# Optimization experiments

Hardware: AMD Instinct MI355X
Metric: run time of the kernel (lower is better)

The kernel has to match this reference:

```python
import jax, jax.numpy as jnp
import numpy as np

B, T, I, H, FUT = 16384, 50, 6, 128, 30


def setup_inputs() -> dict:
    key = jax.random.key(0)
    ks = jax.random.split(key, 10)
    bound = 1.0 / np.sqrt(H)
    u = lambda k, shape: jax.random.uniform(k, shape, jnp.float32, -bound, bound)
    return {
        "history": jax.random.normal(ks[0], (B, T, I), jnp.float32),
        # GRU weights (PyTorch layout: gates stacked [r, z, n])
        "w_ih": u(ks[1], (3 * H, I)),
        "w_hh": u(ks[2], (3 * H, H)),
        "b_ih": u(ks[3], (3 * H,)),
        "b_hh": u(ks[4], (3 * H,)),
        # MLP head: Linear(H,H) -> ReLU -> Linear(H,I)
        "w1": u(ks[5], (H, H)),
        "b1": u(ks[6], (H,)),
        "w2": u(ks[7], (I, H)),
        "b2": u(ks[8], (I,)),
    }


def _gru_cell(h, x, w_ih, w_hh, b_ih, b_hh):
    # PyTorch GRU cell: gates ordered r, z, n
    gi = x @ w_ih.T + b_ih          # (B, 3H)
    gh = h @ w_hh.T + b_hh          # (B, 3H)
    i_r, i_z, i_n = jnp.split(gi, 3, axis=-1)
    h_r, h_z, h_n = jnp.split(gh, 3, axis=-1)
    r = jax.nn.sigmoid(i_r + h_r)
    z = jax.nn.sigmoid(i_z + h_z)
    n = jnp.tanh(i_n + r * h_n)
    return (1.0 - z) * n + z * h


def reference(history, w_ih, w_hh, b_ih, b_hh, w1, b1, w2, b2):
    # --- encode history: scan GRU over time ---
    h0 = jnp.zeros((history.shape[0], H), history.dtype)

    def enc_step(h, x_t):
        return _gru_cell(h, x_t, w_ih, w_hh, b_ih, b_hh), None

    h_last, _ = jax.lax.scan(enc_step, h0, jnp.swapaxes(history, 0, 1))  # (B, H)

    def head(h):
        return jax.nn.relu(h @ w1.T + b1) @ w2.T + b2  # (B, I)

    def dec_step(carry, _):
        h, x = carry
        h = _gru_cell(h, x, w_ih, w_hh, b_ih, b_hh)
        x = head(h)
        return (h, x), x

    x0 = history[:, -1]  # (B, I)
    _, preds = jax.lax.scan(dec_step, (h_last, x0), None, length=FUT)  # (FUT, B, I)
    return jnp.swapaxes(preds, 0, 1)  # (B, FUT, I)
```

## Files before the change

### kernel.cpp

```cpp
#include <hip/hip_runtime.h>

typedef _Float16 half8 __attribute__((ext_vector_type(8)));
typedef float f32x4 __attribute__((ext_vector_type(4)));

#define ROWS 32
#define HP 136
#define HBUFSZ (ROWS * HP)
#define LOG2E 1.442695041f
#define MFMA(a, b, c) __builtin_amdgcn_mfma_f32_16x16x32_f16((a), (b), (c), 0, 0, 0)

__global__ __launch_bounds__(512, 4)
void traj_gru(const float* __restrict__ history,
              const float* __restrict__ w_ih, const float* __restrict__ w_hh,
              const float* __restrict__ b_ih, const float* __restrict__ b_hh,
              const float* __restrict__ w1, const float* __restrict__ b1,
              const float* __restrict__ w2, const float* __restrict__ b2,
              float* __restrict__ out)
{
    __shared__ __align__(16) _Float16 hbuf[2 * HBUFSZ];
    __shared__ __align__(16) _Float16 xhist[50 * ROWS * 8];
    __shared__ __align__(16) _Float16 xdec[ROWS * 8];
    __shared__ __align__(16) _Float16 a1s[ROWS * HP];
    __shared__ __align__(16) _Float16 w2f[4 * 4 * 16 * 8];

    const int tid  = threadIdx.x;
    const int wave = tid >> 6;
    const int lane = tid & 63;
    const int ln16 = lane & 15;
    const int q    = lane >> 4;
    const int rowbase = blockIdx.x * ROWS;
    const int cbase = wave * 16;

    for (int i = tid; i < 2 * HBUFSZ; i += 512) hbuf[i] = (_Float16)0;
    for (int i = tid; i < 50 * ROWS * 8; i += 512) xhist[i] = (_Float16)0;
    for (int i = tid; i < ROWS * 8; i += 512) xdec[i] = (_Float16)0;
    for (int i = tid; i < 4 * 4 * 16 * 8; i += 512) w2f[i] = (_Float16)0;
    __syncthreads();

    for (int idx = tid; idx < ROWS * 300; idx += 512) {
        int r = idx / 300, rem = idx - r * 300;
        int t = rem / 6, c = rem - t * 6;
        xhist[(t * ROWS + r) * 8 + c] = (_Float16)history[(rowbase + r) * 300 + rem];
    }
    for (int idx = tid; idx < 50 * ROWS; idx += 512)
        xhist[idx * 8 + 6] = (_Float16)1.0f;
    for (int idx = tid; idx < ROWS; idx += 512)
        xdec[idx * 8 + 6] = (_Float16)1.0f;
    for (int idx = tid; idx < 6 * 128; idx += 512) {
        int n = idx >> 7, k = idx & 127;
        int kt = k >> 5, qq = (k >> 3) & 3, j = k & 7;
        w2f[((kt * 4 + qq) * 16 + n) * 8 + j] = (_Float16)w2[n * 128 + k];
    }

    half8 Bh[3][4];
    #pragma unroll
    for (int g = 0; g < 3; ++g) {
        float sc = (g < 2) ? -LOG2E : -2.0f * LOG2E;
        #pragma unroll
        for (int kt = 0; kt < 4; ++kt) {
            int n = g * 128 + cbase + ln16;
            const float* p = w_hh + n * 128 + kt * 32 + q * 8;
            half8 v;
            #pragma unroll
            for (int j = 0; j < 8; ++j) v[j] = (_Float16)(p[j] * sc);
            Bh[g][kt] = v;
        }
    }
    half8 Bi[3];
    #pragma unroll
    for (int g = 0; g < 3; ++g) {
        float sc = (g < 2) ? -LOG2E : -2.0f * LOG2E;
        int n = g * 128 + cbase + ln16;
        half8 v;
        #pragma unroll
        for (int j = 0; j < 8; ++j) v[j] = (_Float16)0.0f;
        if (q == 0) {
            #pragma unroll
            for (int j = 0; j < 6; ++j) v[j] = (_Float16)(w_ih[n * 6 + j] * sc);
            v[6] = (_Float16)((b_ih[n] + (g < 2 ? b_hh[n] : 0.0f)) * sc);
        }
        Bi[g] = v;
    }
    const float bhn = b_hh[256 + cbase + ln16] * (-2.0f * LOG2E);
    half8 Bw1[4];
    #pragma unroll
    for (int kt = 0; kt < 4; ++kt) {
        int n = cbase + ln16;
        const float* p = w1 + n * 128 + kt * 32 + q * 8;
        half8 v;
        #pragma unroll
        for (int j = 0; j < 8; ++j) v[j] = (_Float16)p[j];
        Bw1[kt] = v;
    }
    const float b1r = b1[cbase + ln16];
    const float b2r = (ln16 < 6) ? b2[ln16] : 0.0f;

    float hp[2][4] = {};

    __syncthreads();

    auto gru_step = [&](int p, const _Float16* xp) {
        const _Float16* hb = hbuf + p * HBUFSZ;
        _Float16*       hn = hbuf + (p ^ 1) * HBUFSZ;
        #pragma unroll
        for (int mt = 0; mt < 2; ++mt) {
            const _Float16* rp = hb + (mt * 16 + ln16) * HP + q * 8;
            half8 Ax = {0,0,0,0,0,0,0,0};
            if (q == 0) Ax = *(const half8*)(xp + (mt * 16 + ln16) * 8);
            f32x4 ar = {0,0,0,0}, az = {0,0,0,0}, ah = {0,0,0,0}, an = {0,0,0,0};
            half8 Acur = *(const half8*)(rp);
            #pragma unroll
            for (int kt = 0; kt < 4; ++kt) {
                half8 Anext;
                if (kt < 3) Anext = *(const half8*)(rp + (kt + 1) * 32);
                ar = MFMA(Acur, Bh[0][kt], ar);
                az = MFMA(Acur, Bh[1][kt], az);
                ah = MFMA(Acur, Bh[2][kt], ah);
                Acur = Anext;
            }
            ar = MFMA(Ax, Bi[0], ar);
            az = MFMA(Ax, Bi[1], az);
            an = MFMA(Ax, Bi[2], an);
            _Float16* wp = hn + (mt * 16 + q * 4) * HP + cbase + ln16;
            #pragma unroll
            for (int i = 0; i < 4; ++i) {
                float r = __builtin_amdgcn_rcpf(1.0f + __builtin_amdgcn_exp2f(ar[i]));
                float z = __builtin_amdgcn_rcpf(1.0f + __builtin_amdgcn_exp2f(az[i]));
                float t = an[i] + r * (ah[i] + bhn);
                float n = 2.0f * __builtin_amdgcn_rcpf(1.0f + __builtin_amdgcn_exp2f(t)) - 1.0f;
                float h = n + z * (hp[mt][i] - n);
                hp[mt][i] = h;
                wp[i * HP] = (_Float16)h;
            }
        }
        __syncthreads();
    };

    auto head_step = [&](int f, int p) {
        const _Float16* hb = hbuf + p * HBUFSZ;
        #pragma unroll
        for (int mt = 0; mt < 2; ++mt) {
            const _Float16* rp = hb + (mt * 16 + ln16) * HP + q * 8;
            f32x4 a = {0,0,0,0};
            half8 Acur = *(const half8*)(rp);
            #pragma unroll
            for (int kt = 0; kt < 4; ++kt) {
                half8 Anext;
                if (kt < 3) Anext = *(const half8*)(rp + (kt + 1) * 32);
                a = MFMA(Acur, Bw1[kt], a);
                Acur = Anext;
            }
            _Float16* wp = a1s + (mt * 16 + q * 4) * HP + cbase + ln16;
            #pragma unroll
            for (int i = 0; i < 4; ++i) {
                float v = a[i] + b1r;
                v = v > 0.0f ? v : 0.0f;
                wp[i * HP] = (_Float16)v;
            }
        }
        __syncthreads();
        if (wave < 2) {
            f32x4 o = {0,0,0,0};
            #pragma unroll
            for (int kt = 0; kt < 4; ++kt) {
                half8 Aa = *(const half8*)&a1s[(wave * 16 + ln16) * HP + kt * 32 + q * 8];
                half8 Bw = *(const half8*)&w2f[((kt * 4 + q) * 16 + ln16) * 8];
                o = MFMA(Aa, Bw, o);
            }
            if (ln16 < 6) {
                #pragma unroll
                for (int i = 0; i < 4; ++i) {
                    int row = wave * 16 + q * 4 + i;
                    float v = o[i] + b2r;
                    out[(rowbase + row) * 180 + f * 6 + ln16] = v;
                    xdec[row * 8 + ln16] = (_Float16)v;
                }
            }
        }
        __syncthreads();
    };

    int p = 0;
    #pragma unroll 1
    for (int t = 0; t < 50; ++t) { gru_step(p, xhist + t * ROWS * 8); p ^= 1; }
    #pragma unroll 1
    for (int f = 0; f < 30; ++f) {
        gru_step(p, f == 0 ? xhist + 49 * ROWS * 8 : xdec);
        p ^= 1;
        head_step(f, p);
    }
}

extern "C" void kernel_launch(void* const* d_in, const int* in_sizes, int n_in,
                              void* d_out, int out_size, void* d_ws, size_t ws_size,
                              hipStream_t stream) {
    (void)in_sizes; (void)n_in; (void)d_ws; (void)ws_size; (void)out_size;
    traj_gru<<<dim3(16384 / ROWS), dim3(512), 0, stream>>>(
        (const float*)d_in[0], (const float*)d_in[1], (const float*)d_in[2],
        (const float*)d_in[3], (const float*)d_in[4], (const float*)d_in[5],
        (const float*)d_in[6], (const float*)d_in[7], (const float*)d_in[8],
        (float*)d_out);
}
```

Measured before the change: 287.4 us.

## Switch GRU to 32x32x16 MFMA with 4 waves and transposed operand roles

Moves the GRU recurrence from 8 waves of 16x16x32 MFMA to 4 waves of 32x32x16 MFMA. Weights become the A operand and the hidden state the B operand, so each wave computes 32 hidden dims for all 32 rows. It also folds b_hn into an extra MFMA, merges the z and tanh reciprocals into a single rcp, and packs h stores into half4 writes. The head now reloads w1 from global memory each step and adds a staggered s_sleep per block. Register pressure rises with 8 k-tiles of weights per gate and 16-wide accumulators, and w1 is reloaded from global on every decode step.

```diff
diff --git a/kernel.cpp b/kernel.cpp
--- a/kernel.cpp
+++ b/kernel.cpp
@@ -1,15 +1,19 @@
 #include <hip/hip_runtime.h>
 
 typedef _Float16 half8 __attribute__((ext_vector_type(8)));
+typedef _Float16 half4 __attribute__((ext_vector_type(4)));
 typedef float f32x4 __attribute__((ext_vector_type(4)));
+typedef float f32x16 __attribute__((ext_vector_type(16)));
+typedef int int4v __attribute__((ext_vector_type(4)));
 
 #define ROWS 32
 #define HP 136
-#define HBUFSZ (ROWS * HP)
+#define HB (ROWS * HP)
 #define LOG2E 1.442695041f
-#define MFMA(a, b, c) __builtin_amdgcn_mfma_f32_16x16x32_f16((a), (b), (c), 0, 0, 0)
-
-__global__ __launch_bounds__(512, 4)
+#define MFMA32(a,b,c) __builtin_amdgcn_mfma_f32_32x32x16_f16((a),(b),(c),0,0,0)
+#define MFMA16(a,b,c) __builtin_amdgcn_mfma_f32_16x16x32_f16((a),(b),(c),0,0,0)
+
+__global__ __launch_bounds__(256, 2)
 void traj_gru(const float* __restrict__ history,
               const float* __restrict__ w_ih, const float* __restrict__ w_hh,
               const float* __restrict__ b_ih, const float* __restrict__ b_hh,
@@ -17,155 +21,193 @@
               const float* __restrict__ w2, const float* __restrict__ b2,
               float* __restrict__ out)
 {
-    __shared__ __align__(16) _Float16 hbuf[2 * HBUFSZ];
-    __shared__ __align__(16) _Float16 xhist[50 * ROWS * 8];
+    __shared__ __align__(16) _Float16 hbuf[2 * HB];
+    __shared__ __align__(16) _Float16 xhist[50 * ROWS * 6];
     __shared__ __align__(16) _Float16 xdec[ROWS * 8];
-    __shared__ __align__(16) _Float16 a1s[ROWS * HP];
     __shared__ __align__(16) _Float16 w2f[4 * 4 * 16 * 8];
 
     const int tid  = threadIdx.x;
     const int wave = tid >> 6;
     const int lane = tid & 63;
+    const int l31  = lane & 31;
+    const int q2   = lane >> 5;
     const int ln16 = lane & 15;
     const int q    = lane >> 4;
     const int rowbase = blockIdx.x * ROWS;
-    const int cbase = wave * 16;
-
-    for (int i = tid; i < 2 * HBUFSZ; i += 512) hbuf[i] = (_Float16)0;
-    for (int i = tid; i < 50 * ROWS * 8; i += 512) xhist[i] = (_Float16)0;
-    for (int i = tid; i < ROWS * 8; i += 512) xdec[i] = (_Float16)0;
-    for (int i = tid; i < 4 * 4 * 16 * 8; i += 512) w2f[i] = (_Float16)0;
+    const int dim0 = wave * 32 + l31;
+
+    for (int i = tid; i < 2 * HB; i += 256) hbuf[i] = (_Float16)0;
+    for (int i = tid; i < ROWS * 8; i += 256) xdec[i] = (_Float16)0;
+    for (int i = tid; i < 4 * 4 * 16 * 8; i += 256) w2f[i] = (_Float16)0;
     __syncthreads();
-
-    for (int idx = tid; idx < ROWS * 300; idx += 512) {
+    for (int idx = tid; idx < ROWS * 300; idx += 256) {
         int r = idx / 300, rem = idx - r * 300;
         int t = rem / 6, c = rem - t * 6;
-        xhist[(t * ROWS + r) * 8 + c] = (_Float16)history[(rowbase + r) * 300 + rem];
-    }
-    for (int idx = tid; idx < 50 * ROWS; idx += 512)
-        xhist[idx * 8 + 6] = (_Float16)1.0f;
-    for (int idx = tid; idx < ROWS; idx += 512)
-        xdec[idx * 8 + 6] = (_Float16)1.0f;
-    for (int idx = tid; idx < 6 * 128; idx += 512) {
+        xhist[(t * ROWS + r) * 6 + c] = (_Float16)history[(rowbase + r) * 300 + rem];
+    }
+    if (tid < ROWS) { xdec[tid * 8 + 6] = (_Float16)1.0f; xdec[tid * 8 + 7] = (_Float16)1.0f; }
+    for (int idx = tid; idx < 6 * 128; idx += 256) {
         int n = idx >> 7, k = idx & 127;
         int kt = k >> 5, qq = (k >> 3) & 3, j = k & 7;
         w2f[((kt * 4 + qq) * 16 + n) * 8 + j] = (_Float16)w2[n * 128 + k];
     }
 
-    half8 Bh[3][4];
+    half8 Wg[3][8];
     #pragma unroll
     for (int g = 0; g < 3; ++g) {
         float sc = (g < 2) ? -LOG2E : -2.0f * LOG2E;
         #pragma unroll
-        for (int kt = 0; kt < 4; ++kt) {
-            int n = g * 128 + cbase + ln16;
-            const float* p = w_hh + n * 128 + kt * 32 + q * 8;
+        for (int kt = 0; kt < 8; ++kt) {
+            const float* p = w_hh + (g * 128 + dim0) * 128 + kt * 16 + q2 * 8;
             half8 v;
             #pragma unroll
             for (int j = 0; j < 8; ++j) v[j] = (_Float16)(p[j] * sc);
-            Bh[g][kt] = v;
-        }
-    }
-    half8 Bi[3];
+            Wg[g][kt] = v;
+        }
+    }
+    half8 Wx[3];
     #pragma unroll
     for (int g = 0; g < 3; ++g) {
         float sc = (g < 2) ? -LOG2E : -2.0f * LOG2E;
-        int n = g * 128 + cbase + ln16;
-        half8 v;
-        #pragma unroll
-        for (int j = 0; j < 8; ++j) v[j] = (_Float16)0.0f;
-        if (q == 0) {
-            #pragma unroll
-            for (int j = 0; j < 6; ++j) v[j] = (_Float16)(w_ih[n * 6 + j] * sc);
-            v[6] = (_Float16)((b_ih[n] + (g < 2 ? b_hh[n] : 0.0f)) * sc);
-        }
-        Bi[g] = v;
-    }
-    const float bhn = b_hh[256 + cbase + ln16] * (-2.0f * LOG2E);
-    half8 Bw1[4];
-    #pragma unroll
-    for (int kt = 0; kt < 4; ++kt) {
-        int n = cbase + ln16;
-        const float* p = w1 + n * 128 + kt * 32 + q * 8;
-        half8 v;
-        #pragma unroll
-        for (int j = 0; j < 8; ++j) v[j] = (_Float16)p[j];
-        Bw1[kt] = v;
-    }
-    const float b1r = b1[cbase + ln16];
+        half8 v = {0,0,0,0,0,0,0,0};
+        if (q2 == 0) {
+            #pragma unroll
+            for (int j = 0; j < 6; ++j) v[j] = (_Float16)(w_ih[(g * 128 + dim0) * 6 + j] * sc);
+            float b = (g == 0) ? (b_ih[dim0] + b_hh[dim0])
+                    : (g == 1) ? (b_ih[128 + dim0] + b_hh[128 + dim0])
+                               : b_ih[256 + dim0];
+            v[6] = (_Float16)(b * sc);
+        }
+        Wx[g] = v;
+    }
+    half8 Wbh = {0,0,0,0,0,0,0,0};
+    if (q2 == 0) Wbh[7] = (_Float16)(b_hh[256 + dim0] * (-2.0f * LOG2E));
+
     const float b2r = (ln16 < 6) ? b2[ln16] : 0.0f;
 
-    float hp[2][4] = {};
+    float hp[16] = {};
 
     __syncthreads();
 
-    auto gru_step = [&](int p, const _Float16* xp) {
-        const _Float16* hb = hbuf + p * HBUFSZ;
-        _Float16*       hn = hbuf + (p ^ 1) * HBUFSZ;
-        #pragma unroll
-        for (int mt = 0; mt < 2; ++mt) {
-            const _Float16* rp = hb + (mt * 16 + ln16) * HP + q * 8;
-            half8 Ax = {0,0,0,0,0,0,0,0};
-            if (q == 0) Ax = *(const half8*)(xp + (mt * 16 + ln16) * 8);
-            f32x4 ar = {0,0,0,0}, az = {0,0,0,0}, ah = {0,0,0,0}, an = {0,0,0,0};
-            half8 Acur = *(const half8*)(rp);
-            #pragma unroll
-            for (int kt = 0; kt < 4; ++kt) {
-                half8 Anext;
-                if (kt < 3) Anext = *(const half8*)(rp + (kt + 1) * 32);
-                ar = MFMA(Acur, Bh[0][kt], ar);
-                az = MFMA(Acur, Bh[1][kt], az);
-                ah = MFMA(Acur, Bh[2][kt], ah);
-                Acur = Anext;
-            }
-            ar = MFMA(Ax, Bi[0], ar);
-            az = MFMA(Ax, Bi[1], az);
-            an = MFMA(Ax, Bi[2], an);
-            _Float16* wp = hn + (mt * 16 + q * 4) * HP + cbase + ln16;
+    {
+        int ph = blockIdx.x & 3;
+        for (int i = 0; i < ph; ++i) __builtin_amdgcn_s_sleep(13);
+    }
+
+    auto gru_step = [&](int p, int t, bool enc) {
+        const _Float16* hb = hbuf + p * HB;
+        _Float16*       hn = hbuf + (p ^ 1) * HB;
+
+        half8 Bx;
+        if (enc) {
+            int4v d = {0, 0, 0, 0};
+            if (q2 == 0) {
+                const int* xi = (const int*)xhist;
+                int base = (t * ROWS + l31) * 3;
+                d[0] = xi[base]; d[1] = xi[base + 1]; d[2] = xi[base + 2];
+                d[3] = 0x3C003C00;
+            }
+            Bx = __builtin_bit_cast(half8, d);
+        } else {
+            half8 z = {0,0,0,0,0,0,0,0};
+            Bx = (q2 == 0) ? *(const half8*)(xdec + l31 * 8) : z;
+        }
+
+        f32x16 ar = {0,0,0,0,0,0,0,0,0,0,0,0,0,0,0,0};
+        f32x16 az = ar, ah = ar, an = ar;
+        const _Float16* rp = hb + l31 * HP + q2 * 8;
+
+        half8 Bf[4];
+        #pragma unroll
+        for (int kt = 0; kt < 4; ++kt) Bf[kt] = *(const half8*)(rp + kt * 16);
+        #pragma unroll
+        for (int kt = 0; kt < 4; ++kt) {
+            ar = MFMA32(Wg[0][kt], Bf[kt], ar);
+            az = MFMA32(Wg[1][kt], Bf[kt], az);
+            ah = MFMA32(Wg[2][kt], Bf[kt], ah);
+        }
+        #pragma unroll
+        for (int kt = 0; kt < 4; ++kt) Bf[kt] = *(const half8*)(rp + (kt + 4) * 16);
+        #pragma unroll
+        for (int kt = 0; kt < 4; ++kt) {
+            ar = MFMA32(Wg[0][kt + 4], Bf[kt], ar);
+            az = MFMA32(Wg[1][kt + 4], Bf[kt], az);
+            ah = MFMA32(Wg[2][kt + 4], Bf[kt], ah);
+        }
+        ar = MFMA32(Wx[0], Bx, ar);
+        az = MFMA32(Wx[1], Bx, az);
+        an = MFMA32(Wx[2], Bx, an);
+        ah = MFMA32(Wbh, Bx, ah);
+
+        #pragma unroll
+        for (int rq = 0; rq < 4; ++rq) {
+            half4 hv;
             #pragma unroll
             for (int i = 0; i < 4; ++i) {
-                float r = __builtin_amdgcn_rcpf(1.0f + __builtin_amdgcn_exp2f(ar[i]));
-                float z = __builtin_amdgcn_rcpf(1.0f + __builtin_amdgcn_exp2f(az[i]));
-                float t = an[i] + r * (ah[i] + bhn);
-                float n = 2.0f * __builtin_amdgcn_rcpf(1.0f + __builtin_amdgcn_exp2f(t)) - 1.0f;
-                float h = n + z * (hp[mt][i] - n);
-                hp[mt][i] = h;
-                wp[i * HP] = (_Float16)h;
-            }
+                int ri = rq * 4 + i;
+                float er = __builtin_amdgcn_exp2f(ar[ri]);
+                float r  = __builtin_amdgcn_rcpf(1.0f + er);
+                float tt = __builtin_fmaf(r, ah[ri], an[ri]);
+                float et = __builtin_amdgcn_exp2f(tt);
+                float ez = __builtin_amdgcn_exp2f(az[ri]);
+                float d1 = 1.0f + et;
+                float rd = __builtin_amdgcn_rcpf(d1 * (1.0f + ez));
+                float t1 = __builtin_fmaf(-et, ez, ez);
+                float nm = __builtin_fmaf(hp[ri], d1, t1);
+                float h  = nm * rd;
+                hp[ri] = h;
+                hv[i] = (_Float16)h;
+            }
+            *(half4*)(hn + l31 * HP + wave * 32 + rq * 8 + q2 * 4) = hv;
         }
         __syncthreads();
     };
 
     auto head_step = [&](int f, int p) {
-        const _Float16* hb = hbuf + p * HBUFSZ;
-        #pragma unroll
-        for (int mt = 0; mt < 2; ++mt) {
-            const _Float16* rp = hb + (mt * 16 + ln16) * HP + q * 8;
-            f32x4 a = {0,0,0,0};
-            half8 Acur = *(const half8*)(rp);
-            #pragma unroll
-            for (int kt = 0; kt < 4; ++kt) {
-                half8 Anext;
-                if (kt < 3) Anext = *(const half8*)(rp + (kt + 1) * 32);
-                a = MFMA(Acur, Bw1[kt], a);
-                Acur = Anext;
-            }
-            _Float16* wp = a1s + (mt * 16 + q * 4) * HP + cbase + ln16;
+        const _Float16* hb = hbuf + p * HB;
+        _Float16*       a1 = hbuf + (p ^ 1) * HB;
+
+        f32x4 wr[16];
+        const f32x4* pw4 = (const f32x4*)(w1 + dim0 * 128);
+        #pragma unroll
+        for (int kt = 0; kt < 8; ++kt) {
+            wr[2 * kt]     = pw4[kt * 4 + q2 * 2];
+            wr[2 * kt + 1] = pw4[kt * 4 + q2 * 2 + 1];
+        }
+        const _Float16* rp = hb + l31 * HP + q2 * 8;
+        f32x16 a = {0,0,0,0,0,0,0,0,0,0,0,0,0,0,0,0};
+        #pragma unroll
+        for (int kt = 0; kt < 8; ++kt) {
+            half8 wv;
+            #pragma unroll
+            for (int j = 0; j < 4; ++j) { wv[j] = (_Float16)wr[2*kt][j]; wv[4+j] = (_Float16)wr[2*kt+1][j]; }
+            half8 bf = *(const half8*)(rp + kt * 16);
+            a = MFMA32(wv, bf, a);
+        }
+        {
+            half8 bx1 = {0,0,0,0,0,0,0,0}, wb = {0,0,0,0,0,0,0,0};
+            if (q2 == 0) { bx1[0] = (_Float16)1.0f; wb[0] = (_Float16)b1[dim0]; }
+            a = MFMA32(wb, bx1, a);
+        }
+        #pragma unroll
+        for (int rq = 0; rq < 4; ++rq) {
+            half4 v;
             #pragma unroll
             for (int i = 0; i < 4; ++i) {
-                float v = a[i] + b1r;
-                v = v > 0.0f ? v : 0.0f;
-                wp[i * HP] = (_Float16)v;
-            }
+                float x = a[rq * 4 + i];
+                v[i] = (_Float16)(x > 0.0f ? x : 0.0f);
+            }
+            *(half4*)(a1 + l31 * HP + wave * 32 + rq * 8 + q2 * 4) = v;
         }
         __syncthreads();
         if (wave < 2) {
+            const _Float16* ap = a1 + (wave * 16 + ln16) * HP;
             f32x4 o = {0,0,0,0};
             #pragma unroll
             for (int kt = 0; kt < 4; ++kt) {
-                half8 Aa = *(const half8*)&a1s[(wave * 16 + ln16) * HP + kt * 32 + q * 8];
+                half8 Aa = *(const half8*)(ap + kt * 32 + q * 8);
                 half8 Bw = *(const half8*)&w2f[((kt * 4 + q) * 16 + ln16) * 8];
-                o = MFMA(Aa, Bw, o);
+                o = MFMA16(Aa, Bw, o);
             }
             if (ln16 < 6) {
                 #pragma unroll
@@ -182,10 +224,10 @@
 
     int p = 0;
     #pragma unroll 1
-    for (int t = 0; t < 50; ++t) { gru_step(p, xhist + t * ROWS * 8); p ^= 1; }
+    for (int t = 0; t < 50; ++t) { gru_step(p, t, true); p ^= 1; }
     #pragma unroll 1
     for (int f = 0; f < 30; ++f) {
-        gru_step(p, f == 0 ? xhist + 49 * ROWS * 8 : xdec);
+        gru_step(p, f == 0 ? 49 : 0, f == 0);
         p ^= 1;
         head_step(f, p);
     }
@@ -195,7 +237,7 @@
                               void* d_out, int out_size, void* d_ws, size_t ws_size,
                               hipStream_t stream) {
     (void)in_sizes; (void)n_in; (void)d_ws; (void)ws_size; (void)out_size;
-    traj_gru<<<dim3(16384 / ROWS), dim3(512), 0, stream>>>(
+    traj_gru<<<dim3(16384 / ROWS), dim3(256), 0, stream>>>(
         (const float*)d_in[0], (const float*)d_in[1], (const float*)d_in[2],
         (const float*)d_in[3], (const float*)d_in[4], (const float*)d_in[5],
         (const float*)d_in[6], (const float*)d_in[7], (const float*)d_in[8],
```

New measurement: 271.4 us. 5.6% less time.
